# Optimization experiments

Hardware: AMD Instinct MI355X
Metric: run time of the kernel (lower is better)

## Reference

```python
import jax, jax.numpy as jnp
import numpy as np

N_NODES = 100000
N_EDGES = 1600000
IN_DIM = 128
HID = 128
OUT_DIM = 1
EPS = 1e-5
NEG_SLOPE = 0.01


def _glorot(key, shape):
    fan_in = shape[-1]
    return jax.random.normal(key, shape, dtype=jnp.float32) / np.sqrt(fan_in)


def setup_inputs() -> dict:
    key = jax.random.key(0)
    ks = jax.random.split(key, 16)
    x = jax.random.normal(ks[0], (N_NODES, IN_DIM), dtype=jnp.float32)
    edge_index = jax.random.randint(ks[1], (2, N_EDGES), 0, N_NODES, dtype=jnp.int64 if jax.config.jax_enable_x64 else jnp.int32)
    params = {
        'W_in': _glorot(ks[2], (HID, IN_DIM)), 'b_in': jnp.zeros((HID,), jnp.float32),
        # SAGEConv params: lin_l (applied to max-aggregated neighbors, with bias), lin_r (applied to self, no bias)
        'W_l1': _glorot(ks[3], (HID, HID)), 'b_l1': jnp.zeros((HID,), jnp.float32), 'W_r1': _glorot(ks[4], (HID, HID)),
        'W_l2': _glorot(ks[5], (HID, HID)), 'b_l2': jnp.zeros((HID,), jnp.float32), 'W_r2': _glorot(ks[6], (HID, HID)),
        'W_l3': _glorot(ks[7], (HID, HID)), 'b_l3': jnp.zeros((HID,), jnp.float32), 'W_r3': _glorot(ks[8], (HID, HID)),
        'g1': jnp.ones((HID,), jnp.float32), 'be1': jnp.zeros((HID,), jnp.float32),
        'g2': jnp.ones((HID,), jnp.float32), 'be2': jnp.zeros((HID,), jnp.float32),
        'g3': jnp.ones((HID,), jnp.float32), 'be3': jnp.zeros((HID,), jnp.float32),
        'W_fc1': _glorot(ks[9], (HID // 2, HID)), 'b_fc1': jnp.zeros((HID // 2,), jnp.float32),
        'W_fc2': _glorot(ks[10], (OUT_DIM, HID // 2)), 'b_fc2': jnp.zeros((OUT_DIM,), jnp.float32),
    }
    return {'x': x, 'edge_index': edge_index, **params}


def _sage_conv_max(x, src, dst, W_l, b_l, W_r):
    # gather source features per edge, scatter-max into destination nodes
    agg = jax.ops.segment_max(x[src], dst, num_segments=N_NODES)  # [N, H], -inf where no neighbors
    agg = jnp.where(jnp.isfinite(agg), agg, 0.0)
    return agg @ W_l.T + b_l + x @ W_r.T


def _batch_norm(x, gamma, beta):
    mean = x.mean(axis=0)
    var = x.var(axis=0)
    return gamma * (x - mean) * jax.lax.rsqrt(var + EPS) + beta


def _lrelu(x):
    return jax.nn.leaky_relu(x, negative_slope=NEG_SLOPE)


def reference(x, edge_index, W_in, b_in,
              W_l1, b_l1, W_r1, W_l2, b_l2, W_r2, W_l3, b_l3, W_r3,
              g1, be1, g2, be2, g3, be3,
              W_fc1, b_fc1, W_fc2, b_fc2):
    src, dst = edge_index[0], edge_index[1]
    h = x @ W_in.T + b_in
    residual = h
    h = _lrelu(_batch_norm(_sage_conv_max(h, src, dst, W_l1, b_l1, W_r1), g1, be1))
    h = _lrelu(_batch_norm(_sage_conv_max(h, src, dst, W_l2, b_l2, W_r2), g2, be2))
    h = _lrelu(_batch_norm(_sage_conv_max(h, src, dst, W_l3, b_l3, W_r3), g3, be3))
    h = h + residual  # dropout layers are identity in deterministic/eval reference
    h = _lrelu(h @ W_fc1.T + b_fc1)
    return h @ W_fc2.T + b_fc2  # [N, OUT_DIM]
```

## Files before the change

kernel.cpp:

```cpp
#include <hip/hip_runtime.h>
#include <cstdint>
#include <cstddef>

#define HID 128

typedef __bf16 bf16x8 __attribute__((ext_vector_type(8)));
typedef float f32x4 __attribute__((ext_vector_type(4)));

__device__ __forceinline__ float bf2f(uint32_t u) {
    union { uint32_t i; float f; } x; x.i = u << 16; return x.f;
}
__device__ __forceinline__ float bflo(uint32_t p) { return bf2f(p & 0xffffu); }
__device__ __forceinline__ float bfhi(uint32_t p) { return bf2f(p >> 16); }
__device__ __forceinline__ float bfs(const uint16_t* p) { return bf2f((uint32_t)*p); }
__device__ __forceinline__ uint16_t f2bf(float f) {
    union { float f; uint32_t i; } x; x.f = f;
    uint32_t u = x.i;
    return (uint16_t)((u + 0x7fffu + ((u >> 16) & 1u)) >> 16);
}
__device__ __forceinline__ uint32_t pack2(float a, float b) {
    return (uint32_t)f2bf(a) | ((uint32_t)f2bf(b) << 16);
}
__device__ __forceinline__ float lrelu_f(float v) { return v > 0.f ? v : 0.01f * v; }
__device__ __forceinline__ bf16x8 ldfrag(const uint16_t* p) {
    union { uint4 u; bf16x8 b; } c;
    c.u = *(const uint4*)p;
    return c.b;
}

__global__ __launch_bounds__(256) void sentinel_kernel(float* out, int n) {
    int i = blockIdx.x * 256 + threadIdx.x;
    if (i < n) out[i] = 65536.0f;
}

__global__ void detect_e_kernel(const int* __restrict__ ei, int* __restrict__ flagE) {
    int lane = threadIdx.x;
    int w = ei[2 * lane + 1];
    unsigned long long b = __ballot(w != 0);
    if (lane == 0) flagE[0] = (b == 0ULL) ? 1 : 0;
}
__global__ void detect_f_kernel(const uint32_t* __restrict__ x, int* __restrict__ flagF) {
    int lane = threadIdx.x;
    uint32_t e = (x[lane] >> 7) & 0xFFu;
    unsigned long long b = __ballot(e >= 64u && e <= 144u);
    if (lane == 0) flagF[0] = (b == ~0ULL) ? 0 : 1;
}

struct WArgs {
    const void* src[8];
    uint16_t* dst[8];
    int nrows[8];
};
__global__ __launch_bounds__(256) void convert_w(WArgs a, const int* __restrict__ flagF) {
    int mat = blockIdx.x >> 6;
    int idx = ((blockIdx.x & 63) << 8) + threadIdx.x;
    if (idx < a.nrows[mat] * HID) {
        a.dst[mat][idx] = flagF[0] ? f2bf(((const float*)a.src[mat])[idx])
                                   : ((const uint16_t*)a.src[mat])[idx];
    }
}

struct ParamArgs {
    const void* src[14];
    int off[14];
    int cnt[14];
};
__global__ __launch_bounds__(128) void convert_params(ParamArgs pa, float* __restrict__ params,
                                                      const int* __restrict__ flagF) {
    int b = blockIdx.x, t = threadIdx.x;
    if (t < pa.cnt[b]) {
        float v = flagF[0] ? ((const float*)pa.src[b])[t]
                           : bfs(&((const uint16_t*)pa.src[b])[t]);
        params[pa.off[b] + t] = v;
    }
}

__global__ __launch_bounds__(256) void convert_x(const void* __restrict__ x,
                                                 uint32_t* __restrict__ dst,
                                                 const int* __restrict__ flagF, int total2) {
    int i = blockIdx.x * 256 + threadIdx.x;
    if (i >= total2) return;
    if (flagF[0]) {
        float2 v = ((const float2*)x)[i];
        dst[i] = pack2(v.x, v.y);
    } else {
        dst[i] = ((const uint32_t*)x)[i];
    }
}

#define EPB 2048

__global__ __launch_bounds__(256) void bucket_hist(const int* __restrict__ ei,
                                                   const int* __restrict__ flagE,
                                                   int* __restrict__ bcnt, int E, int NBC) {
    __shared__ int cnt[1024];
    int tid = threadIdx.x;
    for (int b = tid; b < NBC; b += 256) cnt[b] = 0;
    __syncthreads();
    int e0 = blockIdx.x * EPB, e1 = min(e0 + EPB, E);
    int isl = flagE[0];
    for (int i = e0 + tid; i < e1; i += 256) {
        int d = isl ? ei[2 * (E + i)] : ei[E + i];
        atomicAdd(&cnt[d >> 10], 1);
    }
    __syncthreads();
    for (int b = tid; b < NBC; b += 256)
        if (cnt[b]) atomicAdd(&bcnt[b], cnt[b]);
}
__global__ __launch_bounds__(1024) void bucket_scan(const int* __restrict__ bcnt,
                                                    int* __restrict__ bstart,
                                                    int* __restrict__ gcur, int NBC, int E) {
    __shared__ int sm[1024];
    int tid = threadIdx.x;
    int v = (tid < NBC) ? bcnt[tid] : 0;
    sm[tid] = v;
    __syncthreads();
    for (int off = 1; off < 1024; off <<= 1) {
        int t = (tid >= off) ? sm[tid - off] : 0;
        __syncthreads();
        sm[tid] += t;
        __syncthreads();
    }
    int ex = sm[tid] - v;
    if (tid < NBC) { bstart[tid] = ex; gcur[tid] = ex; }
    if (tid == 0) bstart[NBC] = E;
}
__global__ __launch_bounds__(256) void bucket_fill(const int* __restrict__ ei,
                                                   const int* __restrict__ flagE,
                                                   int* __restrict__ gcur,
                                                   uint2* __restrict__ bins, int E, int NBC) {
    __shared__ int cnt[1024];
    __shared__ int res[1024];
    int tid = threadIdx.x;
    for (int b = tid; b < NBC; b += 256) cnt[b] = 0;
    __syncthreads();
    int e0 = blockIdx.x * EPB, e1 = min(e0 + EPB, E);
    int isl = flagE[0];
    for (int i = e0 + tid; i < e1; i += 256) {
        int d = isl ? ei[2 * (E + i)] : ei[E + i];
        atomicAdd(&cnt[d >> 10], 1);
    }
    __syncthreads();
    for (int b = tid; b < NBC; b += 256) {
        res[b] = cnt[b] ? atomicAdd(&gcur[b], cnt[b]) : 0;
        cnt[b] = 0;
    }
    __syncthreads();
    for (int i = e0 + tid; i < e1; i += 256) {
        int s = isl ? ei[2 * i] : ei[i];
        int d = isl ? ei[2 * (E + i)] : ei[E + i];
        int b = d >> 10;
        int pos = res[b] + atomicAdd(&cnt[b], 1);
        bins[pos] = make_uint2((uint32_t)s, (uint32_t)d);
    }
}
__global__ __launch_bounds__(256) void csr_build(const uint2* __restrict__ bins,
                                                 const int* __restrict__ bstart,
                                                 int* __restrict__ rowptr,
                                                 int* __restrict__ csr, int M, int E) {
    int b = blockIdx.x;
    int node0 = b << 10;
    int nn = min(1024, M - node0);
    int s = bstart[b], e = bstart[b + 1];
    __shared__ int cnt[1024];
    __shared__ int ofs[1024];
    int tid = threadIdx.x;
    for (int j = tid; j < 1024; j += 256) cnt[j] = 0;
    __syncthreads();
    for (int i = s + tid; i < e; i += 256)
        atomicAdd(&cnt[bins[i].y & 1023], 1);
    __syncthreads();
    if (tid == 0) {
        int run = s;
        for (int j = 0; j < nn; ++j) { ofs[j] = run; run += cnt[j]; }
    }
    __syncthreads();
    for (int j = tid; j < nn; j += 256) rowptr[node0 + j] = ofs[j];
    if (b == 0 && tid == 0) rowptr[M] = E;
    for (int j = tid; j < 1024; j += 256) cnt[j] = 0;
    __syncthreads();
    for (int i = s + tid; i < e; i += 256) {
        uint2 pr = bins[i];
        int d = pr.y & 1023;
        int pos = ofs[d] + atomicAdd(&cnt[d], 1);
        csr[pos] = (int)pr.x;
    }
}

__global__ __launch_bounds__(256) void gather_kernel(const uint4* __restrict__ cur,
                                                     const int* __restrict__ rowptr,
                                                     const int* __restrict__ csr,
                                                     uint4* __restrict__ agg, int M) {
    int gid = blockIdx.x * 256 + threadIdx.x;
    int node = gid >> 4;
    int sl = threadIdx.x & 15;
    if (node >= M) return;
    int b = rowptr[node], e = rowptr[node + 1];
    float m[8];
#pragma unroll
    for (int j = 0; j < 8; ++j) m[j] = -INFINITY;
    int i = b;
    for (; i + 8 <= e; i += 8) {
        uint4 u[8];
#pragma unroll
        for (int t = 0; t < 8; ++t) u[t] = cur[(size_t)csr[i + t] * 16 + sl];
#pragma unroll
        for (int t = 0; t < 8; ++t) {
            uint32_t w[4] = {u[t].x, u[t].y, u[t].z, u[t].w};
#pragma unroll
            for (int j = 0; j < 4; ++j) {
                m[2 * j]     = fmaxf(m[2 * j],     bflo(w[j]));
                m[2 * j + 1] = fmaxf(m[2 * j + 1], bfhi(w[j]));
            }
        }
    }
    for (; i + 4 <= e; i += 4) {
        uint4 u[4];
#pragma unroll
        for (int t = 0; t < 4; ++t) u[t] = cur[(size_t)csr[i + t] * 16 + sl];
#pragma unroll
        for (int t = 0; t < 4; ++t) {
            uint32_t w[4] = {u[t].x, u[t].y, u[t].z, u[t].w};
#pragma unroll
            for (int j = 0; j < 4; ++j) {
                m[2 * j]     = fmaxf(m[2 * j],     bflo(w[j]));
                m[2 * j + 1] = fmaxf(m[2 * j + 1], bfhi(w[j]));
            }
        }
    }
    for (; i < e; ++i) {
        uint4 u0 = cur[(size_t)csr[i] * 16 + sl];
        uint32_t w0[4] = {u0.x, u0.y, u0.z, u0.w};
#pragma unroll
        for (int j = 0; j < 4; ++j) {
            m[2 * j]     = fmaxf(m[2 * j],     bflo(w0[j]));
            m[2 * j + 1] = fmaxf(m[2 * j + 1], bfhi(w0[j]));
        }
    }
    if (b == e) {
#pragma unroll
        for (int j = 0; j < 8; ++j) m[j] = 0.f;
    }
    uint4 o;
    o.x = pack2(m[0], m[1]); o.y = pack2(m[2], m[3]);
    o.z = pack2(m[4], m[5]); o.w = pack2(m[6], m[7]);
    agg[(size_t)node * 16 + sl] = o;
}

template<int N, int NSRC, bool FC2>
__global__ __launch_bounds__(256, 3) void gemm_mfma(
    const uint16_t* __restrict__ A0, const uint16_t* __restrict__ W0,
    const uint16_t* __restrict__ A1, const uint16_t* __restrict__ W1,
    const float* __restrict__ bias, void* __restrict__ out_, int M,
    const float* __restrict__ fc2w)
{
    constexpr int LDT = 72;
    constexpr int WAVES_N = N / 64;
    constexpr int WAVES_M = 4 / WAVES_N;
    constexpr int MT = 8 / WAVES_M;
    constexpr int NT = 4;
    constexpr int NW = N / 32;
    constexpr int CHUNKS = 2 * NSRC;
    __shared__ uint16_t LX[128 * LDT];
    __shared__ uint16_t LW[N * LDT];
    const int tid = threadIdx.x;
    const int wave = tid >> 6, lane = tid & 63;
    const int l15 = lane & 15, lkg = lane >> 4;
    const int wn = (wave % WAVES_N) * 64;
    const int wm = (wave / WAVES_N) * (128 / WAVES_M);
    const int row0 = blockIdx.x * 128;
    const int srow = tid >> 3;
    const int sko = (tid & 7) * 8;

    f32x4 acc[NT][MT];
#pragma unroll
    for (int nt = 0; nt < NT; ++nt)
#pragma unroll
        for (int mt = 0; mt < MT; ++mt) {
            f32x4 z4 = {0.f, 0.f, 0.f, 0.f};
            acc[nt][mt] = z4;
        }

    const uint16_t* Asrc[2] = {A0, NSRC > 1 ? A1 : A0};
    const uint16_t* Wsrc[2] = {W0, NSRC > 1 ? W1 : W0};

    uint4 rx[4], rw[NW];
#pragma unroll
    for (int it = 0; it < 4; ++it) {
        int gr = row0 + srow + it * 32;
        uint4 v = make_uint4(0, 0, 0, 0);
        if (gr < M) v = *(const uint4*)(Asrc[0] + (size_t)gr * HID + sko);
        rx[it] = v;
    }
#pragma unroll
    for (int it = 0; it < NW; ++it)
        rw[it] = *(const uint4*)(Wsrc[0] + (size_t)(srow + it * 32) * HID + sko);

#pragma unroll 1
    for (int c = 0; c < CHUNKS; ++c) {
        __syncthreads();
#pragma unroll
        for (int it = 0; it < 4; ++it)
            *(uint4*)&LX[(srow + it * 32) * LDT + sko] = rx[it];
#pragma unroll
        for (int it = 0; it < NW; ++it)
            *(uint4*)&LW[(srow + it * 32) * LDT + sko] = rw[it];
        __syncthreads();
        if (c + 1 < CHUNKS) {
            int nc = c + 1, src = nc >> 1, kc = nc & 1;
            const uint16_t* Ag = Asrc[src];
#pragma unroll
            for (int it = 0; it < 4; ++it) {
                int gr = row0 + srow + it * 32;
                uint4 v = make_uint4(0, 0, 0, 0);
                if (gr < M) v = *(const uint4*)(Ag + (size_t)gr * HID + kc * 64 + sko);
                rx[it] = v;
            }
            const uint16_t* Wg = Wsrc[src];
#pragma unroll
            for (int it = 0; it < NW; ++it)
                rw[it] = *(const uint4*)(Wg + (size_t)(srow + it * 32) * HID + kc * 64 + sko);
        }
#pragma unroll
        for (int ks = 0; ks < 2; ++ks) {
            bf16x8 xf[MT], wf[NT];
#pragma unroll
            for (int mt = 0; mt < MT; ++mt)
                xf[mt] = ldfrag(&LX[(wm + mt * 16 + l15) * LDT + ks * 32 + lkg * 8]);
#pragma unroll
            for (int nt = 0; nt < NT; ++nt)
                wf[nt] = ldfrag(&LW[(wn + nt * 16 + l15) * LDT + ks * 32 + lkg * 8]);
#pragma unroll
            for (int nt = 0; nt < NT; ++nt)
#pragma unroll
                for (int mt = 0; mt < MT; ++mt)
                    acc[nt][mt] = __builtin_amdgcn_mfma_f32_16x16x32_bf16(
                        wf[nt], xf[mt], acc[nt][mt], 0, 0, 0);
        }
    }

    if constexpr (FC2) {
        float rowdot[MT];
#pragma unroll
        for (int mt = 0; mt < MT; ++mt) rowdot[mt] = 0.f;
#pragma unroll
        for (int nt = 0; nt < NT; ++nt) {
            int n0 = wn + nt * 16 + lkg * 4;
            float b4[4] = {bias[n0], bias[n0 + 1], bias[n0 + 2], bias[n0 + 3]};
            float w4[4] = {fc2w[n0], fc2w[n0 + 1], fc2w[n0 + 2], fc2w[n0 + 3]};
#pragma unroll
            for (int mt = 0; mt < MT; ++mt) {
                f32x4 f = acc[nt][mt];
#pragma unroll
                for (int j = 0; j < 4; ++j)
                    rowdot[mt] = fmaf(lrelu_f(f[j] + b4[j]), w4[j], rowdot[mt]);
            }
        }
        float b2 = fc2w[64];
#pragma unroll
        for (int mt = 0; mt < MT; ++mt) {
            float v = rowdot[mt];
            v += __shfl_xor(v, 16, 64);
            v += __shfl_xor(v, 32, 64);
            int m = row0 + wm + mt * 16 + l15;
            if (lkg == 0 && m < M) ((float*)out_)[m] = v + b2;
        }
    } else {
#pragma unroll
        for (int nt = 0; nt < NT; ++nt) {
            int n0 = wn + nt * 16 + lkg * 4;
            float b0 = bias[n0], b1 = bias[n0 + 1], b2 = bias[n0 + 2], b3 = bias[n0 + 3];
#pragma unroll
            for (int mt = 0; mt < MT; ++mt) {
                int m = row0 + wm + mt * 16 + l15;
                if (m < M) {
                    f32x4 f = acc[nt][mt];
                    ushort4 ov;
                    ov.x = f2bf(f[0] + b0); ov.y = f2bf(f[1] + b1);
                    ov.z = f2bf(f[2] + b2); ov.w = f2bf(f[3] + b3);
                    *(ushort4*)((uint16_t*)out_ + (size_t)m * N + n0) = ov;
                }
            }
        }
    }
}

__global__ __launch_bounds__(256) void bn_stats(const uint32_t* __restrict__ z,
                                                float* __restrict__ stats, int M, int rpb) {
    __shared__ float4 red[256];
    int c2 = threadIdx.x & 63;
    int part = threadIdx.x >> 6;
    int s0 = blockIdx.x * rpb, e0 = min(s0 + rpb, M);
    float sl = 0.f, s2l = 0.f, sh = 0.f, s2h = 0.f;
    for (int r = s0 + part; r < e0; r += 4) {
        uint32_t u = z[(size_t)r * 64 + c2];
        float a = bflo(u), b = bfhi(u);
        sl += a; s2l = fmaf(a, a, s2l);
        sh += b; s2h = fmaf(b, b, s2h);
    }
    red[threadIdx.x] = make_float4(sl, s2l, sh, s2h);
    __syncthreads();
    if (threadIdx.x < 64) {
        float4 v = red[threadIdx.x];
        float4 v1 = red[threadIdx.x + 64], v2 = red[threadIdx.x + 128], v3 = red[threadIdx.x + 192];
        v.x += v1.x + v2.x + v3.x; v.y += v1.y + v2.y + v3.y;
        v.z += v1.z + v2.z + v3.z; v.w += v1.w + v2.w + v3.w;
        int cc = c2 * 2;
        atomicAdd(&stats[cc], v.x);
        atomicAdd(&stats[128 + cc], v.y);
        atomicAdd(&stats[cc + 1], v.z);
        atomicAdd(&stats[129 + cc], v.w);
    }
}
__global__ void bn_finalize(float* stats, const float* __restrict__ g,
                            const float* __restrict__ be, int M) {
    int c = threadIdx.x;
    float mean = stats[c] / (float)M;
    float var = stats[128 + c] / (float)M - mean * mean;
    float sc = g[c] * rsqrtf(var + 1e-5f);
    stats[c] = sc;
    stats[128 + c] = be[c] - mean * sc;
}
__global__ __launch_bounds__(256) void bn_apply(uint32_t* __restrict__ z,
                                                const float* __restrict__ stats, int total2) {
    int i = blockIdx.x * 256 + threadIdx.x;
    if (i >= total2) return;
    int cc = (i & 63) * 2;
    uint32_t u = z[i];
    float a = lrelu_f(fmaf(bflo(u), stats[cc], stats[128 + cc]));
    float b = lrelu_f(fmaf(bfhi(u), stats[cc + 1], stats[129 + cc]));
    z[i] = pack2(a, b);
}
__global__ __launch_bounds__(256) void bn_apply_res(uint32_t* __restrict__ z,
                                                    const uint32_t* __restrict__ h0,
                                                    const float* __restrict__ stats, int total2) {
    int i = blockIdx.x * 256 + threadIdx.x;
    if (i >= total2) return;
    int cc = (i & 63) * 2;
    uint32_t u = z[i], r = h0[i];
    float a = lrelu_f(fmaf(bflo(u), stats[cc], stats[128 + cc])) + bflo(r);
    float b = lrelu_f(fmaf(bfhi(u), stats[cc + 1], stats[129 + cc])) + bfhi(r);
    z[i] = pack2(a, b);
}

extern "C" void kernel_launch(void* const* d_in, const int* in_sizes, int n_in,
                              void* d_out, int out_size, void* d_ws, size_t ws_size,
                              hipStream_t stream) {
    const void* x = d_in[0];
    const int* ei = (const int*)d_in[1];
    const int M = in_sizes[0] / HID;
    const int E = in_sizes[1] / 2;
    const int NBC = (M + 1023) >> 10;
    const int gemm_grid = (M + 127) / 128;

    const size_t FEAT = (size_t)M * HID * 2;
    char* p = (char*)d_ws;
    uint16_t* H0 = (uint16_t*)p; p += FEAT;
    uint16_t* P  = (uint16_t*)p; p += FEAT;
    uint16_t* Q  = (uint16_t*)p; p += FEAT;
    uint16_t* WT = (uint16_t*)p; p += 8 * 16384 * 2;
    float* params = (float*)p; p += 8192;
    int* rowptr  = (int*)p; p += ((size_t)M + 32) * 4;
    int* csr     = (int*)p; p += (size_t)E * 4;
    int* bcnt    = (int*)p; p += 1024 * 4;
    int* bstart  = (int*)p; p += 1056 * 4;
    int* gcur    = (int*)p; p += 1024 * 4;
    float* stats = (float*)p; p += 3 * 256 * 4;
    int* flagE   = (int*)p; p += 128;
    int* flagF   = (int*)p; p += 128;

    const size_t needed = (size_t)(p - (char*)d_ws);
    if (needed > ws_size) {
        sentinel_kernel<<<(out_size + 255) / 256, 256, 0, stream>>>(
            (float*)d_out, out_size);
        return;
    }

    uint16_t* wt[8];
    for (int i = 0; i < 8; ++i) wt[i] = WT + (size_t)i * 16384;

    detect_e_kernel<<<1, 64, 0, stream>>>(ei, flagE);
    detect_f_kernel<<<1, 64, 0, stream>>>((const uint32_t*)x, flagF);

    WArgs wa;
    const int widx[8] = {2, 4, 6, 7, 9, 10, 12, 19};
    for (int i = 0; i < 8; ++i) {
        wa.src[i] = d_in[widx[i]];
        wa.dst[i] = wt[i];
        wa.nrows[i] = (i == 7) ? 64 : 128;
    }
    convert_w<<<512, 256, 0, stream>>>(wa, flagF);

    ParamArgs pa;
    const int pidx[14] = {3, 5, 8, 11, 13, 15, 17, 14, 16, 18, 20, 21, 22, 22};
    const int poff[14] = {0, 128, 256, 384, 512, 640, 768, 896, 1024, 1152, 1280, 1344, 1408, 1409};
    const int pcnt[14] = {128, 128, 128, 128, 128, 128, 128, 128, 128, 128, 64, 64, 1, 0};
    for (int i = 0; i < 14; ++i) { pa.src[i] = d_in[pidx[i]]; pa.off[i] = poff[i]; pa.cnt[i] = pcnt[i]; }
    convert_params<<<14, 128, 0, stream>>>(pa, params, flagF);

    const int total2 = M * (HID / 2);
    const int ew_grid = (total2 + 255) / 256;
    convert_x<<<ew_grid, 256, 0, stream>>>(x, (uint32_t*)Q, flagF, total2);

    hipMemsetAsync(bcnt, 0, 1024 * sizeof(int), stream);
    hipMemsetAsync(stats, 0, 3 * 256 * sizeof(float), stream);
    const int fgrid = (E + EPB - 1) / EPB;
    bucket_hist<<<fgrid, 256, 0, stream>>>(ei, flagE, bcnt, E, NBC);
    bucket_scan<<<1, 1024, 0, stream>>>(bcnt, bstart, gcur, NBC, E);
    bucket_fill<<<fgrid, 256, 0, stream>>>(ei, flagE, gcur, (uint2*)P, E, NBC);
    csr_build<<<NBC, 256, 0, stream>>>((const uint2*)P, bstart, rowptr, csr, M, E);

    const int gather_grid = (M + 15) / 16;
    const int rpb = (M + 255) / 256;

    gemm_mfma<128, 1, false><<<gemm_grid, 256, 0, stream>>>(
        Q, wt[0], nullptr, nullptr, params + 0, H0, M, nullptr);

    uint16_t* wtl[3] = {wt[1], wt[3], wt[5]};
    uint16_t* wtr[3] = {wt[2], wt[4], wt[6]};
    uint16_t* cur = H0;
    uint16_t* dstb[3] = {P, Q, P};
    for (int l = 0; l < 3; ++l) {
        uint16_t* z = dstb[l];
        float* sl = stats + 256 * l;
        gather_kernel<<<gather_grid, 256, 0, stream>>>(
            (const uint4*)cur, rowptr, csr, (uint4*)z, M);
        gemm_mfma<128, 2, false><<<gemm_grid, 256, 0, stream>>>(
            z, wtl[l], cur, wtr[l], params + 128 + l * 128, z, M, nullptr);
        bn_stats<<<256, 256, 0, stream>>>((const uint32_t*)z, sl, M, rpb);
        bn_finalize<<<1, 128, 0, stream>>>(sl, params + 512 + l * 128,
                                           params + 896 + l * 128, M);
        if (l < 2)
            bn_apply<<<ew_grid, 256, 0, stream>>>((uint32_t*)z, sl, total2);
        else
            bn_apply_res<<<ew_grid, 256, 0, stream>>>((uint32_t*)z, (const uint32_t*)H0,
                                                      sl, total2);
        cur = z;
    }

    gemm_mfma<64, 1, true><<<gemm_grid, 256, 0, stream>>>(
        P, wt[7], nullptr, nullptr, params + 1280, (float*)d_out, M, params + 1344);
}
```

Baseline: 727.5 us.

## Read GEMM weight fragments from global memory and fold BN finalize into apply

The GEMM kernel no longer stages weight tiles through shared memory; each wave loads its MFMA weight fragments straight from global (L1/L2-cached) memory. This halves LDS usage, and the launch-bounds occupancy hint is raised from 3 to 4 blocks. The separate bn_finalize launch is removed: bn_apply recomputes the per-channel scale and shift from raw stats in every thread, trading one kernel launch for redundant rsqrt work and extra stats reads. Direct global fragment loads are uncoalesced and may add latency to the MFMA loop.

```diff
diff --git a/kernel.cpp b/kernel.cpp
--- a/kernel.cpp
+++ b/kernel.cpp
@@ -248,7 +248,7 @@
 }
 
 template<int N, int NSRC, bool FC2>
-__global__ __launch_bounds__(256, 3) void gemm_mfma(
+__global__ __launch_bounds__(256, 4) void gemm_mfma(
     const uint16_t* __restrict__ A0, const uint16_t* __restrict__ W0,
     const uint16_t* __restrict__ A1, const uint16_t* __restrict__ W1,
     const float* __restrict__ bias, void* __restrict__ out_, int M,
@@ -259,10 +259,8 @@
     constexpr int WAVES_M = 4 / WAVES_N;
     constexpr int MT = 8 / WAVES_M;
     constexpr int NT = 4;
-    constexpr int NW = N / 32;
     constexpr int CHUNKS = 2 * NSRC;
     __shared__ uint16_t LX[128 * LDT];
-    __shared__ uint16_t LW[N * LDT];
     const int tid = threadIdx.x;
     const int wave = tid >> 6, lane = tid & 63;
     const int l15 = lane & 15, lkg = lane >> 4;
@@ -284,7 +282,7 @@
     const uint16_t* Asrc[2] = {A0, NSRC > 1 ? A1 : A0};
     const uint16_t* Wsrc[2] = {W0, NSRC > 1 ? W1 : W0};
 
-    uint4 rx[4], rw[NW];
+    uint4 rx[4];
 #pragma unroll
     for (int it = 0; it < 4; ++it) {
         int gr = row0 + srow + it * 32;
@@ -292,19 +290,15 @@
         if (gr < M) v = *(const uint4*)(Asrc[0] + (size_t)gr * HID + sko);
         rx[it] = v;
     }
-#pragma unroll
-    for (int it = 0; it < NW; ++it)
-        rw[it] = *(const uint4*)(Wsrc[0] + (size_t)(srow + it * 32) * HID + sko);
 
 #pragma unroll 1
     for (int c = 0; c < CHUNKS; ++c) {
+        const int csrc = c >> 1, ckc = c & 1;
+        const uint16_t* Wg = Wsrc[csrc];
         __syncthreads();
 #pragma unroll
         for (int it = 0; it < 4; ++it)
             *(uint4*)&LX[(srow + it * 32) * LDT + sko] = rx[it];
-#pragma unroll
-        for (int it = 0; it < NW; ++it)
-            *(uint4*)&LW[(srow + it * 32) * LDT + sko] = rw[it];
         __syncthreads();
         if (c + 1 < CHUNKS) {
             int nc = c + 1, src = nc >> 1, kc = nc & 1;
@@ -316,10 +310,6 @@
                 if (gr < M) v = *(const uint4*)(Ag + (size_t)gr * HID + kc * 64 + sko);
                 rx[it] = v;
             }
-            const uint16_t* Wg = Wsrc[src];
-#pragma unroll
-            for (int it = 0; it < NW; ++it)
-                rw[it] = *(const uint4*)(Wg + (size_t)(srow + it * 32) * HID + kc * 64 + sko);
         }
 #pragma unroll
         for (int ks = 0; ks < 2; ++ks) {
@@ -329,7 +319,8 @@
                 xf[mt] = ldfrag(&LX[(wm + mt * 16 + l15) * LDT + ks * 32 + lkg * 8]);
 #pragma unroll
             for (int nt = 0; nt < NT; ++nt)
-                wf[nt] = ldfrag(&LW[(wn + nt * 16 + l15) * LDT + ks * 32 + lkg * 8]);
+                wf[nt] = ldfrag(Wg + (size_t)(wn + nt * 16 + l15) * HID +
+                                ckc * 64 + ks * 32 + lkg * 8);
 #pragma unroll
             for (int nt = 0; nt < NT; ++nt)
 #pragma unroll
@@ -412,34 +403,44 @@
         atomicAdd(&stats[129 + cc], v.w);
     }
 }
-__global__ void bn_finalize(float* stats, const float* __restrict__ g,
-                            const float* __restrict__ be, int M) {
-    int c = threadIdx.x;
-    float mean = stats[c] / (float)M;
-    float var = stats[128 + c] / (float)M - mean * mean;
+__device__ __forceinline__ float2 bn_coeff(const float* stats, const float* g,
+                                           const float* be, int c, float invM) {
+    float mean = stats[c] * invM;
+    float var = stats[128 + c] * invM - mean * mean;
     float sc = g[c] * rsqrtf(var + 1e-5f);
-    stats[c] = sc;
-    stats[128 + c] = be[c] - mean * sc;
+    return make_float2(sc, be[c] - mean * sc);
 }
 __global__ __launch_bounds__(256) void bn_apply(uint32_t* __restrict__ z,
-                                                const float* __restrict__ stats, int total2) {
+                                                const float* __restrict__ stats,
+                                                const float* __restrict__ g,
+                                                const float* __restrict__ be,
+                                                int M, int total2) {
     int i = blockIdx.x * 256 + threadIdx.x;
     if (i >= total2) return;
+    float invM = 1.f / (float)M;
     int cc = (i & 63) * 2;
+    float2 k0 = bn_coeff(stats, g, be, cc, invM);
+    float2 k1 = bn_coeff(stats, g, be, cc + 1, invM);
     uint32_t u = z[i];
-    float a = lrelu_f(fmaf(bflo(u), stats[cc], stats[128 + cc]));
-    float b = lrelu_f(fmaf(bfhi(u), stats[cc + 1], stats[129 + cc]));
+    float a = lrelu_f(fmaf(bflo(u), k0.x, k0.y));
+    float b = lrelu_f(fmaf(bfhi(u), k1.x, k1.y));
     z[i] = pack2(a, b);
 }
 __global__ __launch_bounds__(256) void bn_apply_res(uint32_t* __restrict__ z,
                                                     const uint32_t* __restrict__ h0,
-                                                    const float* __restrict__ stats, int total2) {
+                                                    const float* __restrict__ stats,
+                                                    const float* __restrict__ g,
+                                                    const float* __restrict__ be,
+                                                    int M, int total2) {
     int i = blockIdx.x * 256 + threadIdx.x;
     if (i >= total2) return;
+    float invM = 1.f / (float)M;
     int cc = (i & 63) * 2;
+    float2 k0 = bn_coeff(stats, g, be, cc, invM);
+    float2 k1 = bn_coeff(stats, g, be, cc + 1, invM);
     uint32_t u = z[i], r = h0[i];
-    float a = lrelu_f(fmaf(bflo(u), stats[cc], stats[128 + cc])) + bflo(r);
-    float b = lrelu_f(fmaf(bfhi(u), stats[cc + 1], stats[129 + cc])) + bfhi(r);
+    float a = lrelu_f(fmaf(bflo(u), k0.x, k0.y)) + bflo(r);
+    float b = lrelu_f(fmaf(bfhi(u), k1.x, k1.y)) + bfhi(r);
     z[i] = pack2(a, b);
 }
 
@@ -523,18 +524,18 @@
     for (int l = 0; l < 3; ++l) {
         uint16_t* z = dstb[l];
         float* sl = stats + 256 * l;
+        const float* gg = params + 512 + l * 128;
+        const float* bb = params + 896 + l * 128;
         gather_kernel<<<gather_grid, 256, 0, stream>>>(
             (const uint4*)cur, rowptr, csr, (uint4*)z, M);
         gemm_mfma<128, 2, false><<<gemm_grid, 256, 0, stream>>>(
             z, wtl[l], cur, wtr[l], params + 128 + l * 128, z, M, nullptr);
         bn_stats<<<256, 256, 0, stream>>>((const uint32_t*)z, sl, M, rpb);
-        bn_finalize<<<1, 128, 0, stream>>>(sl, params + 512 + l * 128,
-                                           params + 896 + l * 128, M);
         if (l < 2)
-            bn_apply<<<ew_grid, 256, 0, stream>>>((uint32_t*)z, sl, total2);
+            bn_apply<<<ew_grid, 256, 0, stream>>>((uint32_t*)z, sl, gg, bb, M, total2);
         else
             bn_apply_res<<<ew_grid, 256, 0, stream>>>((uint32_t*)z, (const uint32_t*)H0,
-                                                      sl, total2);
+                                                      sl, gg, bb, M, total2);
         cur = z;
     }
 
```

Result: no change. 719.7 us (-1.1%).
